# Performance work log

Hardware: AMD Instinct MI355X
Metric: run time of the kernel (lower is better)

Reference implementation:

```python
import jax, jax.numpy as jnp
import numpy as np

N = 50000   # nodes
D = 128     # input_dim
E = 1600000 # edges
K = 100     # out_nodes


def setup_inputs() -> dict:
    key = jax.random.key(0)
    ks = jax.random.split(key, 9)
    x = jax.random.normal(ks[0], (N, D), dtype=jnp.float32)
    edge_index = jax.random.randint(ks[1], (2, E), 0, N, dtype=jnp.int64)
    # PyG GCNConv params: Linear(in,out,bias=False) weight + separate bias
    s = 1.0 / np.sqrt(D)
    W1 = jax.random.uniform(ks[2], (D, D), jnp.float32, -s, s)
    b1 = jnp.zeros((D,), jnp.float32)
    W2 = jax.random.uniform(ks[3], (D, D), jnp.float32, -s, s)
    b2 = jnp.zeros((D,), jnp.float32)
    Wa = jax.random.uniform(ks[4], (D, K), jnp.float32, -s, s)
    ba = jax.random.uniform(ks[5], (K,), jnp.float32, -s, s)
    return {"x": x, "edge_index": edge_index, "W1": W1, "b1": b1,
            "W2": W2, "b2": b2, "Wa": Wa, "ba": ba}


def _gcn_conv(x, src, dst, norm, W, b, n_nodes):
    # PyG GCNConv: h = x @ W; aggregate D^-1/2 (A+I) D^-1/2 h; add bias
    h = x @ W                                  # [N, D]
    msg = h[src] * norm[:, None]               # [E+N, D] gather + scale
    agg = jax.ops.segment_sum(msg, dst, num_segments=n_nodes)  # scatter-add
    return agg + b


def reference(x, edge_index, W1, b1, W2, b2, Wa, ba):
    n = x.shape[0]
    loop = jnp.arange(n, dtype=edge_index.dtype)
    src = jnp.concatenate([edge_index[0], loop])   # add self-loops
    dst = jnp.concatenate([edge_index[1], loop])
    deg = jnp.zeros((n,), x.dtype).at[dst].add(1.0)
    dinv = jnp.where(deg > 0, jax.lax.rsqrt(deg), 0.0)
    norm = dinv[src] * dinv[dst]                   # [E+N]

    h = _gcn_conv(x, src, dst, norm, W1, b1, n)
    h = jax.nn.relu(h)
    h = _gcn_conv(h, src, dst, norm, W2, b2, n)
    s = jax.nn.softmax(h @ Wa + ba, axis=1)        # [N, K]
    return s
```

## Files before the change

### kernel.cpp

```cpp
#include <hip/hip_runtime.h>

#define D 128
#define KOUT 100
#define CHUNK 4096
#define BCAP 12288

typedef __attribute__((ext_vector_type(8))) short short8;
typedef __attribute__((ext_vector_type(4))) float floatx4;

__device__ inline float bf_lo(unsigned int u) { return __uint_as_float(u << 16); }
__device__ inline float bf_hi(unsigned int u) { return __uint_as_float(u & 0xFFFF0000u); }

__device__ inline unsigned int bf_round(float a) {
    unsigned int ua = __float_as_uint(a);
    return (ua + 0x7FFFu + ((ua >> 16) & 1u)) >> 16;
}
__device__ inline unsigned int pack_bf(float a, float b) {
    return bf_round(a) | (bf_round(b) << 16);
}


__launch_bounds__(256)
__global__ void bucket_pass1(const int* __restrict__ ei, int E, int nbuck, int cap,
                             int* __restrict__ bcur, unsigned int* __restrict__ bdata) {
    __shared__ int hist[256];
    __shared__ int sc[256];
    __shared__ int pfx[256];
    __shared__ int cur[256];
    __shared__ int gbase[256];
    __shared__ unsigned int lbuf[CHUNK];
    __shared__ unsigned char bkt[CHUNK];

    int tid = threadIdx.x;
    int base = blockIdx.x * CHUNK;
    int cnt = E - base; if (cnt > CHUNK) cnt = CHUNK;

    hist[tid] = 0;
    __syncthreads();

    int src[CHUNK / 256];
    int dst[CHUNK / 256];
#pragma unroll
    for (int q = 0; q < CHUNK / 256; q++) {
        int li = tid + q * 256;
        if (li < cnt) {
            src[q] = ei[base + li];
            dst[q] = ei[E + base + li];
            atomicAdd(&hist[dst[q] >> 8], 1);
        }
    }
    __syncthreads();

    int v = hist[tid];
    sc[tid] = v;
    __syncthreads();
    for (int off = 1; off < 256; off <<= 1) {
        int t = (tid >= off) ? sc[tid - off] : 0;
        __syncthreads();
        sc[tid] += t;
        __syncthreads();
    }
    int excl = sc[tid] - v;
    pfx[tid] = excl;
    cur[tid] = excl;
    gbase[tid] = 0;
    if (tid < nbuck && v > 0) gbase[tid] = atomicAdd(&bcur[tid], v);
    __syncthreads();

#pragma unroll
    for (int q = 0; q < CHUNK / 256; q++) {
        int li = tid + q * 256;
        if (li < cnt) {
            int b = dst[q] >> 8;
            int p = atomicAdd(&cur[b], 1);
            lbuf[p] = (unsigned int)src[q] | ((unsigned int)(dst[q] & 255) << 24);
            bkt[p] = (unsigned char)b;
        }
    }
    __syncthreads();

    for (int p = tid; p < cnt; p += 256) {
        int b = bkt[p];
        bdata[(size_t)b * cap + gbase[b] + (p - pfx[b])] = lbuf[p];
    }
}


__launch_bounds__(256)
__global__ void bucket_build(const unsigned int* __restrict__ bdata, const int* __restrict__ bcur,
                             int cap, int* __restrict__ deg, float* __restrict__ dinv,
                             int* __restrict__ rowptr, int* __restrict__ csr, int n, int nbuck) {
    __shared__ unsigned int lbuf[BCAP];
    __shared__ int cnts[256];
    __shared__ int sc[256];
    __shared__ int cur[256];
    __shared__ int bbase;

    int b = blockIdx.x, tid = threadIdx.x;
    if (tid == 0) bbase = 0;
    cnts[tid] = 0;
    __syncthreads();

    int part = 0;
    for (int t = tid; t < b; t += 256) part += bcur[t];
#pragma unroll
    for (int off = 32; off > 0; off >>= 1) part += __shfl_down(part, off);
    if ((tid & 63) == 0 && part != 0) atomicAdd(&bbase, part);

    int cnt = bcur[b];
    for (int e = tid; e < cnt; e += 256) {
        unsigned int u = bdata[(size_t)b * cap + e];
        lbuf[e] = u;
        atomicAdd(&cnts[u >> 24], 1);
    }
    __syncthreads();

    int v = cnts[tid];
    sc[tid] = v;
    __syncthreads();
    for (int off = 1; off < 256; off <<= 1) {
        int t = (tid >= off) ? sc[tid - off] : 0;
        __syncthreads();
        sc[tid] += t;
        __syncthreads();
    }
    int gstart = bbase + (sc[tid] - v);
    int node = b * 256 + tid;
    if (node < n) {
        deg[node] = v + 1;
        dinv[node] = rsqrtf((float)(v + 1));
        rowptr[node] = gstart;
    }
    cur[tid] = gstart;
    __syncthreads();

    for (int e = tid; e < cnt; e += 256) {
        unsigned int u = lbuf[e];
        int pos = atomicAdd(&cur[u >> 24], 1);
        csr[pos] = (int)(u & 0xFFFFFFu);
    }
}


__global__ void prep_frag_kernel(const float* __restrict__ W1, const float* __restrict__ W2,
                                 const float* __restrict__ Wa, const float* __restrict__ ba,
                                 unsigned short* __restrict__ Wf1, unsigned short* __restrict__ Wf2,
                                 unsigned short* __restrict__ WfA, float* __restrict__ bpad) {
    int idx = blockIdx.x * blockDim.x + threadIdx.x;
    if (idx < 3 * 16384) {
        int m = idx / 16384;
        int e = idx & 16383;
        int j = e & 7, lane = (e >> 3) & 63, ct = (e >> 9) & 7, kt = e >> 12;
        int k = kt * 32 + (lane >> 4) * 8 + j;
        int col = ct * 16 + (lane & 15);
        float val;
        unsigned short* dst;
        if (m == 0)      { val = W1[k * 128 + col]; dst = Wf1; }
        else if (m == 1) { val = W2[k * 128 + col]; dst = Wf2; }
        else             { val = (col < KOUT) ? Wa[k * KOUT + col] : 0.f; dst = WfA; }
        dst[e] = (unsigned short)bf_round(val);
    }
    if (idx < 128) bpad[idx] = (idx < KOUT) ? ba[idx] : 0.f;
}


__launch_bounds__(256)
__global__ void gemm_mfma_kernel(const void* __restrict__ Xin, const unsigned short* __restrict__ Wf,
                                 const float* __restrict__ bias, void* __restrict__ Y,
                                 int nrows, int in_bf16, int out_mode) {
    __shared__ float lds_f[64 * 130];
    unsigned short* lds_h = (unsigned short*)lds_f;
    unsigned int* lds_u = (unsigned int*)lds_f;

    int tid = threadIdx.x;
    int w = tid >> 6, lane = tid & 63;
    int quad = lane >> 4, m16 = lane & 15;
    int r0 = blockIdx.x * 64;

    if (!in_bf16) {
        int row = tid >> 2, cg = tid & 3;
        bool valid = (r0 + row) < nrows;
        const float4* Xr = (const float4*)Xin + (size_t)(r0 + row) * 32 + cg * 8;
#pragma unroll
        for (int j = 0; j < 8; j++) {
            float4 v = valid ? Xr[j] : make_float4(0.f, 0.f, 0.f, 0.f);
            int c = cg * 32 + j * 4;
            lds_u[row * 68 + (c >> 1)]     = pack_bf(v.x, v.y);
            lds_u[row * 68 + (c >> 1) + 1] = pack_bf(v.z, v.w);
        }
        __syncthreads();
    }

    floatx4 acc[8];
#pragma unroll
    for (int ct = 0; ct < 8; ct++) acc[ct] = (floatx4){0.f, 0.f, 0.f, 0.f};

    int arow = r0 + w * 16 + m16;
    if (arow > nrows - 1) arow = nrows - 1;
    const unsigned int* Xb = (const unsigned int*)Xin;

    const short8* Wf8 = (const short8*)Wf;
#pragma unroll
    for (int kt = 0; kt < 4; kt++) {
        short8 a;
        if (in_bf16) {
            a = *(const short8*)(Xb + (size_t)arow * 64 + kt * 16 + quad * 4);
        } else {
            a = *(const short8*)(lds_h + (w * 16 + m16) * 136 + kt * 32 + quad * 8);
        }
#pragma unroll
        for (int ct = 0; ct < 8; ct++) {
            short8 b = Wf8[(kt * 8 + ct) * 64 + lane];
            acc[ct] = __builtin_amdgcn_mfma_f32_16x16x32_bf16(a, b, acc[ct], 0, 0, 0);
        }
    }

    if (out_mode == 1) {
        __syncthreads();
#pragma unroll
        for (int ct = 0; ct < 8; ct++) {
#pragma unroll
            for (int r = 0; r < 4; r++) {
                int rl = w * 16 + quad * 4 + r;
                lds_f[rl * 130 + ct * 16 + m16] = acc[ct][r];
            }
        }
        __syncthreads();
        unsigned int* Yb = (unsigned int*)Y;
        for (int r = 0; r < 16; r++) {
            int row = r0 + w * 16 + r;
            if (row < nrows) {
                float lo = lds_f[(w * 16 + r) * 130 + 2 * lane];
                float hi = lds_f[(w * 16 + r) * 130 + 2 * lane + 1];
                Yb[(size_t)row * 64 + lane] = pack_bf(lo, hi);
            }
        }
    } else {
        float bb[8];
#pragma unroll
        for (int ct = 0; ct < 8; ct++) bb[ct] = bias[ct * 16 + m16];
        float* Yf = (float*)Y;
#pragma unroll
        for (int r = 0; r < 4; r++) {
            int row = r0 + w * 16 + quad * 4 + r;
            float vv[8];
            float mx = -1e30f;
#pragma unroll
            for (int ct = 0; ct < 8; ct++) {
                int col = ct * 16 + m16;
                vv[ct] = (col < KOUT) ? acc[ct][r] + bb[ct] : -1e30f;
                mx = fmaxf(mx, vv[ct]);
            }
#pragma unroll
            for (int off = 1; off < 16; off <<= 1) mx = fmaxf(mx, __shfl_xor(mx, off));
            float se = 0.f;
#pragma unroll
            for (int ct = 0; ct < 8; ct++) {
                vv[ct] = (vv[ct] > -1e29f) ? __expf(vv[ct] - mx) : 0.f;
                se += vv[ct];
            }
#pragma unroll
            for (int off = 1; off < 16; off <<= 1) se += __shfl_xor(se, off);
            float inv = 1.f / se;
            if (row < nrows) {
#pragma unroll
                for (int ct = 0; ct < 8; ct++) {
                    int col = ct * 16 + m16;
                    if (col < KOUT) Yf[(size_t)row * KOUT + col] = vv[ct] * inv;
                }
            }
        }
    }
}


__launch_bounds__(256)
__global__ void aggregate_kernel(const uint4* __restrict__ Hb4, const int* __restrict__ csr,
                                 const int* __restrict__ rowptr, const int* __restrict__ deg,
                                 const float* __restrict__ dinv, const float* __restrict__ bias,
                                 unsigned int* __restrict__ Ob, int n, int do_relu) {
    int wid = threadIdx.x >> 6, lane = threadIdx.x & 63;
    int g = lane >> 4, c = lane & 15;
    int i = blockIdx.x * 4 + wid;
    if (i >= n) return;

    float di = dinv[i];
    float acc[8];
    {
        uint4 sv = Hb4[(size_t)i * 16 + c];
        float sl = (g == 0) ? di * di : 0.f;
        unsigned int su[4] = {sv.x, sv.y, sv.z, sv.w};
#pragma unroll
        for (int t = 0; t < 4; t++) {
            acc[2 * t]     = bf_lo(su[t]) * sl;
            acc[2 * t + 1] = bf_hi(su[t]) * sl;
        }
    }

    const int* cp = csr + rowptr[i];
    int cnt = deg[i] - 1;
    for (int e = 0; e < cnt; e += 16) {
        int s[4];
        uint4 v[4];
        float wgt[4];
#pragma unroll
        for (int u = 0; u < 4; u++) {
            int idx = e + u * 4 + g;
            s[u] = (idx < cnt) ? cp[idx] : i;
        }
#pragma unroll
        for (int u = 0; u < 4; u++) v[u] = Hb4[(size_t)s[u] * 16 + c];
#pragma unroll
        for (int u = 0; u < 4; u++) {
            int idx = e + u * 4 + g;
            wgt[u] = (idx < cnt) ? dinv[s[u]] * di : 0.f;
        }
#pragma unroll
        for (int u = 0; u < 4; u++) {
            unsigned int uu[4] = {v[u].x, v[u].y, v[u].z, v[u].w};
#pragma unroll
            for (int t = 0; t < 4; t++) {
                acc[2 * t]     = fmaf(bf_lo(uu[t]), wgt[u], acc[2 * t]);
                acc[2 * t + 1] = fmaf(bf_hi(uu[t]), wgt[u], acc[2 * t + 1]);
            }
        }
    }

#pragma unroll
    for (int j = 0; j < 8; j++) {
        acc[j] += __shfl_xor(acc[j], 16);
        acc[j] += __shfl_xor(acc[j], 32);
    }

    float2 bb = ((const float2*)bias)[c * 4 + g];
    float fx = acc[g * 2]     + bb.x;
    float fy = acc[g * 2 + 1] + bb.y;
    if (do_relu) { fx = fmaxf(fx, 0.f); fy = fmaxf(fy, 0.f); }
    Ob[(size_t)i * 64 + c * 4 + g] = pack_bf(fx, fy);
}


extern "C" void kernel_launch(void* const* d_in, const int* in_sizes, int n_in,
                              void* d_out, int out_size, void* d_ws, size_t ws_size,
                              hipStream_t stream) {
    const float* x  = (const float*)d_in[0];
    const int*   ei = (const int*)d_in[1];
    const float* W1 = (const float*)d_in[2];
    const float* b1 = (const float*)d_in[3];
    const float* W2 = (const float*)d_in[4];
    const float* b2 = (const float*)d_in[5];
    const float* Wa = (const float*)d_in[6];
    const float* ba = (const float*)d_in[7];
    float* out = (float*)d_out;

    int N = in_sizes[0] / D;
    int E = in_sizes[1] / 2;

    int nbuck = (N + 255) >> 8;
    int cap = ((E / nbuck) + 2048 + 63) & ~63;

    char* w = (char*)d_ws;
    size_t off = 0;
    auto carve = [&](size_t bytes) -> void* {
        void* p = w + off;
        off = (off + bytes + 255) & ~(size_t)255;
        return p;
    };
    int*   deg    = (int*)carve((size_t)N * 4);
    float* dinv   = (float*)carve((size_t)N * 4);
    int*   rowptr = (int*)carve((size_t)N * 4);
    int*   bcur   = (int*)carve(256 * 4);
    unsigned int* bdata = (unsigned int*)carve((size_t)nbuck * cap * 4);
    int*   csr    = (int*)carve((size_t)E * 4);
    unsigned short* Wf1 = (unsigned short*)carve(16384 * 2);
    unsigned short* Wf2 = (unsigned short*)carve(16384 * 2);
    unsigned short* WfA = (unsigned short*)carve(16384 * 2);
    float* bpad   = (float*)carve(512);
    unsigned int* HbA = (unsigned int*)carve((size_t)N * 64 * 4);
    unsigned int* HbB = (unsigned int*)carve((size_t)N * 64 * 4);
    (void)ws_size; (void)n_in; (void)out_size;

    int nbNode4 = (N + 3) / 4;
    int nbGemm = (N + 63) / 64;
    int nbP1 = (E + CHUNK - 1) / CHUNK;

    (void)hipMemsetAsync(bcur, 0, 256 * 4, stream);
    bucket_pass1<<<nbP1, 256, 0, stream>>>(ei, E, nbuck, cap, bcur, bdata);
    bucket_build<<<nbuck, 256, 0, stream>>>(bdata, bcur, cap, deg, dinv, rowptr, csr, N, nbuck);
    prep_frag_kernel<<<192, 256, 0, stream>>>(W1, W2, Wa, ba, Wf1, Wf2, WfA, bpad);

    gemm_mfma_kernel<<<nbGemm, 256, 0, stream>>>(x, Wf1, nullptr, HbA, N, 0, 1);
    aggregate_kernel<<<nbNode4, 256, 0, stream>>>((const uint4*)HbA, csr, rowptr, deg, dinv, b1, HbB, N, 1);
    gemm_mfma_kernel<<<nbGemm, 256, 0, stream>>>(HbB, Wf2, nullptr, HbA, N, 1, 1);
    aggregate_kernel<<<nbNode4, 256, 0, stream>>>((const uint4*)HbA, csr, rowptr, deg, dinv, b2, HbB, N, 0);
    gemm_mfma_kernel<<<nbGemm, 256, 0, stream>>>(HbB, WfA, bpad, out, N, 1, 2);
}
```

Before: 277.4 us.

## Prescale GEMM output by dinv and drop per-edge weight loads in aggregation

```diff
diff --git a/kernel.cpp b/kernel.cpp
--- a/kernel.cpp
+++ b/kernel.cpp
@@ -3,7 +3,6 @@
 #define D 128
 #define KOUT 100
 #define CHUNK 4096
-#define BCAP 12288
 
 typedef __attribute__((ext_vector_type(8))) short short8;
 typedef __attribute__((ext_vector_type(4))) float floatx4;
@@ -90,7 +89,6 @@
 __global__ void bucket_build(const unsigned int* __restrict__ bdata, const int* __restrict__ bcur,
                              int cap, int* __restrict__ deg, float* __restrict__ dinv,
                              int* __restrict__ rowptr, int* __restrict__ csr, int n, int nbuck) {
-    __shared__ unsigned int lbuf[BCAP];
     __shared__ int cnts[256];
     __shared__ int sc[256];
     __shared__ int cur[256];
@@ -108,11 +106,8 @@
     if ((tid & 63) == 0 && part != 0) atomicAdd(&bbase, part);
 
     int cnt = bcur[b];
-    for (int e = tid; e < cnt; e += 256) {
-        unsigned int u = bdata[(size_t)b * cap + e];
-        lbuf[e] = u;
-        atomicAdd(&cnts[u >> 24], 1);
-    }
+    const unsigned int* p = bdata + (size_t)b * cap;
+    for (int e = tid; e < cnt; e += 256) atomicAdd(&cnts[p[e] >> 24], 1);
     __syncthreads();
 
     int v = cnts[tid];
@@ -135,7 +130,7 @@
     __syncthreads();
 
     for (int e = tid; e < cnt; e += 256) {
-        unsigned int u = lbuf[e];
+        unsigned int u = p[e];
         int pos = atomicAdd(&cur[u >> 24], 1);
         csr[pos] = (int)(u & 0xFFFFFFu);
     }
@@ -145,7 +140,9 @@
 __global__ void prep_frag_kernel(const float* __restrict__ W1, const float* __restrict__ W2,
                                  const float* __restrict__ Wa, const float* __restrict__ ba,
                                  unsigned short* __restrict__ Wf1, unsigned short* __restrict__ Wf2,
-                                 unsigned short* __restrict__ WfA, float* __restrict__ bpad) {
+                                 unsigned short* __restrict__ WfA, float* __restrict__ bpad,
+                                 int* __restrict__ bcur,
+                                 unsigned int* __restrict__ zrowA, unsigned int* __restrict__ zrowB) {
     int idx = blockIdx.x * blockDim.x + threadIdx.x;
     if (idx < 3 * 16384) {
         int m = idx / 16384;
@@ -161,13 +158,15 @@
         dst[e] = (unsigned short)bf_round(val);
     }
     if (idx < 128) bpad[idx] = (idx < KOUT) ? ba[idx] : 0.f;
+    if (idx < 256) bcur[idx] = 0;
+    if (idx < 64) { zrowA[idx] = 0u; zrowB[idx] = 0u; }
 }
 
 
 __launch_bounds__(256)
 __global__ void gemm_mfma_kernel(const void* __restrict__ Xin, const unsigned short* __restrict__ Wf,
-                                 const float* __restrict__ bias, void* __restrict__ Y,
-                                 int nrows, int in_bf16, int out_mode) {
+                                 const float* __restrict__ bias, const float* __restrict__ oscale,
+                                 void* __restrict__ Y, int nrows, int in_bf16, int out_mode) {
     __shared__ float lds_f[64 * 130];
     unsigned short* lds_h = (unsigned short*)lds_f;
     unsigned int* lds_u = (unsigned int*)lds_f;
@@ -230,8 +229,9 @@
         for (int r = 0; r < 16; r++) {
             int row = r0 + w * 16 + r;
             if (row < nrows) {
-                float lo = lds_f[(w * 16 + r) * 130 + 2 * lane];
-                float hi = lds_f[(w * 16 + r) * 130 + 2 * lane + 1];
+                float sc = oscale ? oscale[row] : 1.f;
+                float lo = lds_f[(w * 16 + r) * 130 + 2 * lane] * sc;
+                float hi = lds_f[(w * 16 + r) * 130 + 2 * lane + 1] * sc;
                 Yb[(size_t)row * 64 + lane] = pack_bf(lo, hi);
             }
         }
@@ -288,12 +288,12 @@
     float acc[8];
     {
         uint4 sv = Hb4[(size_t)i * 16 + c];
-        float sl = (g == 0) ? di * di : 0.f;
         unsigned int su[4] = {sv.x, sv.y, sv.z, sv.w};
+        if (g != 0) { su[0] = su[1] = su[2] = su[3] = 0u; }
 #pragma unroll
         for (int t = 0; t < 4; t++) {
-            acc[2 * t]     = bf_lo(su[t]) * sl;
-            acc[2 * t + 1] = bf_hi(su[t]) * sl;
+            acc[2 * t]     = bf_lo(su[t]);
+            acc[2 * t + 1] = bf_hi(su[t]);
         }
     }
 
@@ -302,26 +302,20 @@
     for (int e = 0; e < cnt; e += 16) {
         int s[4];
         uint4 v[4];
-        float wgt[4];
 #pragma unroll
         for (int u = 0; u < 4; u++) {
             int idx = e + u * 4 + g;
-            s[u] = (idx < cnt) ? cp[idx] : i;
+            s[u] = (idx < cnt) ? cp[idx] : n;
         }
 #pragma unroll
         for (int u = 0; u < 4; u++) v[u] = Hb4[(size_t)s[u] * 16 + c];
-#pragma unroll
-        for (int u = 0; u < 4; u++) {
-            int idx = e + u * 4 + g;
-            wgt[u] = (idx < cnt) ? dinv[s[u]] * di : 0.f;
-        }
 #pragma unroll
         for (int u = 0; u < 4; u++) {
             unsigned int uu[4] = {v[u].x, v[u].y, v[u].z, v[u].w};
 #pragma unroll
             for (int t = 0; t < 4; t++) {
-                acc[2 * t]     = fmaf(bf_lo(uu[t]), wgt[u], acc[2 * t]);
-                acc[2 * t + 1] = fmaf(bf_hi(uu[t]), wgt[u], acc[2 * t + 1]);
+                acc[2 * t]     += bf_lo(uu[t]);
+                acc[2 * t + 1] += bf_hi(uu[t]);
             }
         }
     }
@@ -333,8 +327,8 @@
     }
 
     float2 bb = ((const float2*)bias)[c * 4 + g];
-    float fx = acc[g * 2]     + bb.x;
-    float fy = acc[g * 2 + 1] + bb.y;
+    float fx = acc[g * 2]     * di + bb.x;
+    float fy = acc[g * 2 + 1] * di + bb.y;
     if (do_relu) { fx = fmaxf(fx, 0.f); fy = fmaxf(fy, 0.f); }
     Ob[(size_t)i * 64 + c * 4 + g] = pack_bf(fx, fy);
 }
@@ -376,22 +370,22 @@
     unsigned short* Wf2 = (unsigned short*)carve(16384 * 2);
     unsigned short* WfA = (unsigned short*)carve(16384 * 2);
     float* bpad   = (float*)carve(512);
-    unsigned int* HbA = (unsigned int*)carve((size_t)N * 64 * 4);
-    unsigned int* HbB = (unsigned int*)carve((size_t)N * 64 * 4);
+    unsigned int* HbA = (unsigned int*)carve((size_t)(N + 1) * 64 * 4);
+    unsigned int* HbB = (unsigned int*)carve((size_t)(N + 1) * 64 * 4);
     (void)ws_size; (void)n_in; (void)out_size;
 
     int nbNode4 = (N + 3) / 4;
     int nbGemm = (N + 63) / 64;
     int nbP1 = (E + CHUNK - 1) / CHUNK;
 
-    (void)hipMemsetAsync(bcur, 0, 256 * 4, stream);
+    prep_frag_kernel<<<192, 256, 0, stream>>>(W1, W2, Wa, ba, Wf1, Wf2, WfA, bpad,
+                                              bcur, HbA + (size_t)N * 64, HbB + (size_t)N * 64);
     bucket_pass1<<<nbP1, 256, 0, stream>>>(ei, E, nbuck, cap, bcur, bdata);
     bucket_build<<<nbuck, 256, 0, stream>>>(bdata, bcur, cap, deg, dinv, rowptr, csr, N, nbuck);
-    prep_frag_kernel<<<192, 256, 0, stream>>>(W1, W2, Wa, ba, Wf1, Wf2, WfA, bpad);
-
-    gemm_mfma_kernel<<<nbGemm, 256, 0, stream>>>(x, Wf1, nullptr, HbA, N, 0, 1);
+
+    gemm_mfma_kernel<<<nbGemm, 256, 0, stream>>>(x, Wf1, nullptr, dinv, HbA, N, 0, 1);
     aggregate_kernel<<<nbNode4, 256, 0, stream>>>((const uint4*)HbA, csr, rowptr, deg, dinv, b1, HbB, N, 1);
-    gemm_mfma_kernel<<<nbGemm, 256, 0, stream>>>(HbB, Wf2, nullptr, HbA, N, 1, 1);
+    gemm_mfma_kernel<<<nbGemm, 256, 0, stream>>>(HbB, Wf2, nullptr, dinv, HbA, N, 1, 1);
     aggregate_kernel<<<nbNode4, 256, 0, stream>>>((const uint4*)HbA, csr, rowptr, deg, dinv, b2, HbB, N, 0);
-    gemm_mfma_kernel<<<nbGemm, 256, 0, stream>>>(HbB, WfA, bpad, out, N, 1, 2);
-}
+    gemm_mfma_kernel<<<nbGemm, 256, 0, stream>>>(HbB, WfA, bpad, nullptr, out, N, 1, 2);
+}
```

Measured after the change: 269.4 us. -2.9%, faster.
